# Kernel tuning notes

Hardware: AMD Instinct MI355X
Metric: run time of the kernel (lower is better)

The kernel has to match this reference:

```python
import jax, jax.numpy as jnp
import numpy as np

XLIM = 10.0
N_BINS = 200
LATTICE = 12.42
N_O, N_H = 64, 128
T, R = 1000, 8


def setup_inputs() -> dict:
    key = jax.random.key(0)
    k1, k2 = jax.random.split(key)
    n = N_O + N_H
    stacked_radii = jax.random.uniform(k1, (T, R, n, 3), dtype=jnp.float32) * LATTICE
    lattices = jnp.full((3,), LATTICE, dtype=jnp.float32)
    gt_rdf = jax.random.uniform(k2, (3, N_BINS), dtype=jnp.float32)
    idx_O = jnp.arange(N_O, dtype=jnp.int32)
    idx_H = jnp.arange(N_H, dtype=jnp.int32) + N_O
    return {"stacked_radii": stacked_radii, "lattices": lattices,
            "gt_rdf": gt_rdf, "idx_O": idx_O, "idx_H": idx_H}


def reference(stacked_radii, lattices, gt_rdf, idx_O, idx_H):
    bins = jnp.linspace(1e-6, XLIM, N_BINS + 1, dtype=jnp.float32)
    # np.histogram normalization: rho * (4/3)pi (r_hi^3 - r_lo^3)
    shell = (4.0 / 3.0) * np.pi * (bins[1:] ** 3 - bins[:-1] ** 3)
    vol = jnp.prod(lattices)
    # wrap positions into the box (data_seq / L % 1 * L)
    x = stacked_radii / lattices % 1.0 * lattices
    x = jnp.transpose(x, (1, 0, 2, 3))  # [R, T, N, 3]

    def pair_rdf(x_rep, i0, i1):
        x0 = x_rep[:, i0]  # [T, n0, 3]
        x1 = x_rep[:, i1]  # [T, n1, 3]
        # all-pairs minimum-image distance under PBC
        delta = jnp.abs(x0[:, :, None, :] - x1[:, None, :, :])  # [T, n0, n1, 3]
        delta = jnp.where(delta > 0.5 * lattices, delta - lattices, delta)
        d = jnp.sqrt(jnp.sum(delta ** 2, axis=-1)).ravel()
        n_pairs = d.shape[0]  # includes zeros, matches original rho
        mask = (d != 0.0) & (d >= bins[0]) & (d <= bins[-1])
        bidx = jnp.clip(jnp.searchsorted(bins, d, side='right') - 1, 0, N_BINS - 1)
        hist = jax.ops.segment_sum(mask.astype(jnp.float32), bidx, num_segments=N_BINS)
        rho = n_pairs / vol
        return hist / (rho * shell)  # [N_BINS]

    pairs = [(idx_O, idx_O), (idx_H, idx_H), (idx_H, idx_O)]  # OO, HH, HO
    # sequential over replicas (like the original python loop) to bound memory
    rdfs = [jax.lax.map(lambda xr, i0=i0, i1=i1: pair_rdf(xr, i0, i1), x)
            for (i0, i1) in pairs]  # each [R, N_BINS]
    maes = jnp.stack([XLIM * jnp.mean(jnp.abs(r - g), axis=-1)
                      for r, g in zip(rdfs, gt_rdf)], axis=0)  # [3, R]
    max_maes = jnp.max(maes, axis=0)  # [R]
    rdf_stack = jnp.concatenate(rdfs, axis=-1)  # [R, 3*N_BINS]
    return rdf_stack, max_maes
```

## Files before the change

kernel.cpp:

```cpp
#include <hip/hip_runtime.h>
#include <math.h>

#define NUM_T   1000
#define NUM_R   8
#define NBINS   200
#define FPB     2
#define TTSZ    224
#define TYSTR   218
#define NCOL    8
#define HWORDS  2616

__device__ __forceinline__ float approx_sqrt(float x) {
    float r; asm("v_sqrt_f32 %0, %1" : "=v"(r) : "v"(x)); return r;
}
__device__ __forceinline__ float fract_(float x) {
#if __has_builtin(__builtin_amdgcn_fractf)
    return __builtin_amdgcn_fractf(x);
#else
    return x - floorf(x);
#endif
}

__global__ __launch_bounds__(256) void rdf_hist_kernel(
    const float* __restrict__ radii,
    const float* __restrict__ lat,
    unsigned int* __restrict__ gh)
{
    #pragma clang fp contract(off)
    __shared__ float4 posOx[96], posH0[96], posH1[96];
    __shared__ float TT[TTSZ];
    __shared__ unsigned int hist[HWORDS];

    const int tid = threadIdx.x;

    if (tid < TTSZ) {
        float v;
        if (tid <= 200) {
            float b;
            if (tid < NBINS) {
                const double step = (10.0 - 1e-6) / 200.0;
                b = (float)(1e-6 + (double)tid * step);
            } else {
                b = __uint_as_float(__float_as_uint(10.0f) + 1u);
            }
            unsigned lo = 0u, hi = 0x7F800000u;
            while (lo < hi) {
                unsigned mid = (lo + hi) >> 1;
                if (sqrtf(__uint_as_float(mid)) >= b) hi = mid; else lo = mid + 1;
            }
            v = __uint_as_float(lo);
        } else {
            v = __uint_as_float(0x7F800000u);
        }
        TT[tid] = v;
    }
    for (int i = tid; i < HWORDS; i += 256) hist[i] = 0u;

    const float Lx = lat[0], Ly = lat[1], Lz = lat[2];
    __syncthreads();

    const int col = tid & (NCOL - 1);

#define PAIR(PI, PJ, TBASE, W)                                               \
    {                                                                        \
        float tx = (PI).x - (PJ).x;                                          \
        float ty = (PI).y - (PJ).y;                                          \
        float tz = (PI).z - (PJ).z;                                          \
        float ax = fminf(fabsf(tx), Lx - fabsf(tx));                         \
        float ay = fminf(fabsf(ty), Ly - fabsf(ty));                         \
        float az = fminf(fabsf(tz), Lz - fabsf(tz));                         \
        float s  = (ax*ax + ay*ay) + az*az;                                  \
        float z  = approx_sqrt(s * 400.0f);                                  \
        int   k  = (int)z;                                                   \
        float m  = fract_(z);                                                \
        bool amb = fabsf(m - 0.5f) > 0.49980f;                               \
        if (__builtin_expect(__any(amb), 0)) {                               \
            float tlo = TT[k], thi = TT[k + 1];                              \
            k += ((s >= thi) ? 1 : 0) - ((s < tlo) ? 1 : 0);                 \
            if (k < 0) k = 216;                                              \
        }                                                                    \
        int w = (TBASE) + ((k >> 1) << 3);                                   \
        unsigned val = (unsigned)(W) << ((k & 1) << 4);                      \
        atomicAdd(&hist[w], val);                                            \
    }

    const int rep   = blockIdx.x & (NUM_R - 1);
    const int chunk = blockIdx.x / NUM_R;
    const int l     = tid & 63;
    const int q     = tid >> 6;
    const int tbOO  = col;
    const int tbHH  = col + 109 * NCOL;
    const int tbHO  = col + 218 * NCOL;

    float rvx = 0.f, rvy = 0.f, rvz = 0.f;
    {
        const float* s0 = radii + ((size_t)(chunk * FPB) * NUM_R + rep) * (192 * 3);
        if (tid < 192) { rvx = s0[tid*3+0]; rvy = s0[tid*3+1]; rvz = s0[tid*3+2]; }
    }

    #pragma unroll 1
    for (int f = 0; f < FPB; ++f) {
        __syncthreads();
        if (tid < 192) {
            float ux = rvx / Lx; ux -= floorf(ux);
            float uy = rvy / Ly; uy -= floorf(uy);
            float uz = rvz / Lz; uz -= floorf(uz);
            float4 p = make_float4(ux*Lx, uy*Ly, uz*Lz, 0.0f);
            if (tid < 64)       { posOx[tid] = p;  if (tid < 32) posOx[tid+64] = p; }
            else if (tid < 128) { int h = tid-64;  posH0[h] = p; if (h < 32) posH0[h+64] = p; }
            else                { int h = tid-128; posH1[h] = p; if (h < 32) posH1[h+64] = p; }
        }
        __syncthreads();

        if (f + 1 < FPB && tid < 192) {
            const float* s1 = radii + ((size_t)(chunk * FPB + f + 1) * NUM_R + rep) * (192 * 3);
            rvx = s1[tid*3+0]; rvy = s1[tid*3+1]; rvz = s1[tid*3+2];
        }

        const float4 piO = posOx[l];
        const float4 pi0 = posH0[l];
        const float4 pi1 = posH1[l];
        const int jb = l + q + 1;

        #pragma unroll
        for (int it = 0; it < 7; ++it) { float4 pj = posOx[jb + 4*it]; PAIR(piO, pj, tbOO, 2u); }
        if (q < 3 || l < 32)           { float4 pj = posOx[jb + 28];   PAIR(piO, pj, tbOO, 2u); }

        #pragma unroll
        for (int it = 0; it < 7; ++it) { float4 pj = posH0[jb + 4*it]; PAIR(pi0, pj, tbHH, 2u); }
        if (q < 3 || l < 32)           { float4 pj = posH0[jb + 28];   PAIR(pi0, pj, tbHH, 2u); }

        #pragma unroll
        for (int it = 0; it < 7; ++it) { float4 pj = posH1[jb + 4*it]; PAIR(pi1, pj, tbHH, 2u); }
        if (q < 3 || l < 32)           { float4 pj = posH1[jb + 28];   PAIR(pi1, pj, tbHH, 2u); }

        #pragma unroll 4
        for (int jj = 0; jj < 16; ++jj) {
            float4 pj = posH1[q * 16 + jj];
            PAIR(pi0, pj, tbHH, 2u);
        }
        #pragma unroll 4
        for (int jj = 0; jj < 16; ++jj) {
            float4 pj = posOx[q * 16 + jj];
            PAIR(pi0, pj, tbHO, 1u);
            PAIR(pi1, pj, tbHO, 1u);
        }
    }
#undef PAIR

    __syncthreads();
    for (int idx = tid; idx < 3 * NBINS; idx += 256) {
        const int p    = idx / 200;
        const int b    = idx - p * 200;
        const int pr   = p * TYSTR + b;
        const int base = (pr >> 1) << 3;
        const int sh   = (b & 1) << 4;
        const int c0   = idx & (NCOL - 1);
        unsigned sum = 0;
        #pragma unroll
        for (int c = 0; c < NCOL; ++c) {
            unsigned wrd = hist[base + ((c0 + c) & (NCOL - 1))];
            sum += (wrd >> sh) & 0xFFFFu;
        }
        if (sum) atomicAdd(&gh[rep * 3 * NBINS + idx], sum);
    }
}

__global__ __launch_bounds__(256) void rdf_final_kernel(
    const unsigned int* __restrict__ gh,
    const float* __restrict__ gt,
    const float* __restrict__ lat,
    float* __restrict__ out)
{
    #pragma clang fp contract(off)
    const int rep = blockIdx.x;
    const int tid = threadIdx.x;
    __shared__ float bins[NBINS + 1];
    __shared__ float red[256];

    for (int i = tid; i <= NBINS; i += 256) {
        const double step = (10.0 - 1e-6) / 200.0;
        bins[i] = (i == NBINS) ? 10.0f : (float)(1e-6 + (double)i * step);
    }
    __syncthreads();

    const float vol = (lat[0] * lat[1]) * lat[2];
    const float C   = 4.18879020478639053f;
    const int npairs[3] = { NUM_T*64*64, NUM_T*128*128, NUM_T*128*64 };

    float maxmae = -3.0e38f;
    for (int p = 0; p < 3; ++p) {
        float diff = 0.0f;
        if (tid < NBINS) {
            float b0 = bins[tid], b1 = bins[tid + 1];
            float shell = C * (b1*b1*b1 - b0*b0*b0);
            float rho = (float)npairs[p] / vol;
            float g = (float)gh[(rep*3 + p)*NBINS + tid] / (rho * shell);
            out[rep*3*NBINS + p*NBINS + tid] = g;
            diff = fabsf(g - gt[p*NBINS + tid]);
        }
        red[tid] = diff;
        __syncthreads();
        for (int s = 128; s > 0; s >>= 1) {
            if (tid < s) red[tid] += red[tid + s];
            __syncthreads();
        }
        if (tid == 0) {
            float mae = 10.0f * (red[0] / 200.0f);
            if (mae > maxmae) maxmae = mae;
        }
        __syncthreads();
    }
    if (tid == 0) out[NUM_R*3*NBINS + rep] = maxmae;
}

extern "C" void kernel_launch(void* const* d_in, const int* in_sizes, int n_in,
                              void* d_out, int out_size, void* d_ws, size_t ws_size,
                              hipStream_t stream) {
    const float* radii = (const float*)d_in[0];
    const float* lat   = (const float*)d_in[1];
    const float* gt    = (const float*)d_in[2];
    unsigned int* gh   = (unsigned int*)d_ws;

    hipMemsetAsync(gh, 0, NUM_R * 3 * NBINS * sizeof(unsigned int), stream);

    dim3 grid(NUM_R * (NUM_T / FPB));
    hipLaunchKernelGGL(rdf_hist_kernel, grid, dim3(256), 0, stream,
                       radii, lat, gh);
    hipLaunchKernelGGL(rdf_final_kernel, dim3(NUM_R), dim3(256), 0, stream,
                       gh, gt, lat, (float*)d_out);
}
```

Before: 101.0 us.

## Use 32-bit histogram words with fewer copies and readlane broadcast for cross pairs

Replaces the packed 16-bit-per-bin, 8-copy shared histogram with full 32-bit counters, one per bin, replicated in 4 column copies. This removes the shift/mask packing and lets the final reduction read one uint4 per bin. The cross-pair loops (H0-H1 and H-O) now take the j-particle coordinates from registers with readlane broadcasts instead of LDS loads, using a wave-uniform q. Fewer histogram copies may raise LDS atomic contention, in exchange for simpler address arithmetic and less LDS traffic.

```diff
diff --git a/kernel.cpp b/kernel.cpp
--- a/kernel.cpp
+++ b/kernel.cpp
@@ -6,9 +6,9 @@
 #define NBINS   200
 #define FPB     2
 #define TTSZ    224
-#define TYSTR   218
-#define NCOL    8
-#define HWORDS  2616
+#define TYSTR   217
+#define NCOL    4
+#define HWORDS  (3*TYSTR*NCOL)
 
 __device__ __forceinline__ float approx_sqrt(float x) {
     float r; asm("v_sqrt_f32 %0, %1" : "=v"(r) : "v"(x)); return r;
@@ -19,6 +19,9 @@
 #else
     return x - floorf(x);
 #endif
+}
+__device__ __forceinline__ float rlanef(float v, int sidx) {
+    return __uint_as_float(__builtin_amdgcn_readlane(__float_as_uint(v), sidx));
 }
 
 __global__ __launch_bounds__(256) void rdf_hist_kernel(
@@ -29,7 +32,7 @@
     #pragma clang fp contract(off)
     __shared__ float4 posOx[96], posH0[96], posH1[96];
     __shared__ float TT[TTSZ];
-    __shared__ unsigned int hist[HWORDS];
+    __shared__ __align__(16) unsigned int hist[HWORDS];
 
     const int tid = threadIdx.x;
 
@@ -61,11 +64,8 @@
 
     const int col = tid & (NCOL - 1);
 
-#define PAIR(PI, PJ, TBASE, W)                                               \
+#define PTAIL(TB, W)                                                         \
     {                                                                        \
-        float tx = (PI).x - (PJ).x;                                          \
-        float ty = (PI).y - (PJ).y;                                          \
-        float tz = (PI).z - (PJ).z;                                          \
         float ax = fminf(fabsf(tx), Lx - fabsf(tx));                         \
         float ay = fminf(fabsf(ty), Ly - fabsf(ty));                         \
         float az = fminf(fabsf(tz), Lz - fabsf(tz));                         \
@@ -79,18 +79,32 @@
             k += ((s >= thi) ? 1 : 0) - ((s < tlo) ? 1 : 0);                 \
             if (k < 0) k = 216;                                              \
         }                                                                    \
-        int w = (TBASE) + ((k >> 1) << 3);                                   \
-        unsigned val = (unsigned)(W) << ((k & 1) << 4);                      \
-        atomicAdd(&hist[w], val);                                            \
+        atomicAdd(&hist[(TB) + (k << 2)], (W));                              \
+    }
+
+#define PAIRV(PI, PJ, TB, W)                                                 \
+    {                                                                        \
+        float tx = (PI).x - (PJ).x;                                          \
+        float ty = (PI).y - (PJ).y;                                          \
+        float tz = (PI).z - (PJ).z;                                          \
+        PTAIL(TB, W)                                                         \
+    }
+#define PAIRS(PI, SX, SY, SZ, TB, W)                                         \
+    {                                                                        \
+        float tx = (PI).x - (SX);                                            \
+        float ty = (PI).y - (SY);                                            \
+        float tz = (PI).z - (SZ);                                            \
+        PTAIL(TB, W)                                                         \
     }
 
     const int rep   = blockIdx.x & (NUM_R - 1);
     const int chunk = blockIdx.x / NUM_R;
     const int l     = tid & 63;
     const int q     = tid >> 6;
+    const int qu    = __builtin_amdgcn_readfirstlane(q);
     const int tbOO  = col;
-    const int tbHH  = col + 109 * NCOL;
-    const int tbHO  = col + 218 * NCOL;
+    const int tbHH  = col + (TYSTR << 2);
+    const int tbHO  = col + (2 * TYSTR << 2);
 
     float rvx = 0.f, rvy = 0.f, rvz = 0.f;
     {
@@ -123,45 +137,41 @@
         const int jb = l + q + 1;
 
         #pragma unroll
-        for (int it = 0; it < 7; ++it) { float4 pj = posOx[jb + 4*it]; PAIR(piO, pj, tbOO, 2u); }
-        if (q < 3 || l < 32)           { float4 pj = posOx[jb + 28];   PAIR(piO, pj, tbOO, 2u); }
+        for (int it = 0; it < 7; ++it) { float4 pj = posOx[jb + 4*it]; PAIRV(piO, pj, tbOO, 2u); }
+        if (q < 3 || l < 32)           { float4 pj = posOx[jb + 28];   PAIRV(piO, pj, tbOO, 2u); }
 
         #pragma unroll
-        for (int it = 0; it < 7; ++it) { float4 pj = posH0[jb + 4*it]; PAIR(pi0, pj, tbHH, 2u); }
-        if (q < 3 || l < 32)           { float4 pj = posH0[jb + 28];   PAIR(pi0, pj, tbHH, 2u); }
+        for (int it = 0; it < 7; ++it) { float4 pj = posH0[jb + 4*it]; PAIRV(pi0, pj, tbHH, 2u); }
+        if (q < 3 || l < 32)           { float4 pj = posH0[jb + 28];   PAIRV(pi0, pj, tbHH, 2u); }
 
         #pragma unroll
-        for (int it = 0; it < 7; ++it) { float4 pj = posH1[jb + 4*it]; PAIR(pi1, pj, tbHH, 2u); }
-        if (q < 3 || l < 32)           { float4 pj = posH1[jb + 28];   PAIR(pi1, pj, tbHH, 2u); }
+        for (int it = 0; it < 7; ++it) { float4 pj = posH1[jb + 4*it]; PAIRV(pi1, pj, tbHH, 2u); }
+        if (q < 3 || l < 32)           { float4 pj = posH1[jb + 28];   PAIRV(pi1, pj, tbHH, 2u); }
 
         #pragma unroll 4
         for (int jj = 0; jj < 16; ++jj) {
-            float4 pj = posH1[q * 16 + jj];
-            PAIR(pi0, pj, tbHH, 2u);
+            const int idx = qu * 16 + jj;
+            float sx = rlanef(pi1.x, idx), sy = rlanef(pi1.y, idx), sz = rlanef(pi1.z, idx);
+            PAIRS(pi0, sx, sy, sz, tbHH, 2u);
         }
         #pragma unroll 4
         for (int jj = 0; jj < 16; ++jj) {
-            float4 pj = posOx[q * 16 + jj];
-            PAIR(pi0, pj, tbHO, 1u);
-            PAIR(pi1, pj, tbHO, 1u);
-        }
-    }
-#undef PAIR
+            const int idx = qu * 16 + jj;
+            float sx = rlanef(piO.x, idx), sy = rlanef(piO.y, idx), sz = rlanef(piO.z, idx);
+            PAIRS(pi0, sx, sy, sz, tbHO, 1u);
+            PAIRS(pi1, sx, sy, sz, tbHO, 1u);
+        }
+    }
+#undef PAIRV
+#undef PAIRS
+#undef PTAIL
 
     __syncthreads();
     for (int idx = tid; idx < 3 * NBINS; idx += 256) {
-        const int p    = idx / 200;
-        const int b    = idx - p * 200;
-        const int pr   = p * TYSTR + b;
-        const int base = (pr >> 1) << 3;
-        const int sh   = (b & 1) << 4;
-        const int c0   = idx & (NCOL - 1);
-        unsigned sum = 0;
-        #pragma unroll
-        for (int c = 0; c < NCOL; ++c) {
-            unsigned wrd = hist[base + ((c0 + c) & (NCOL - 1))];
-            sum += (wrd >> sh) & 0xFFFFu;
-        }
+        const int p = idx / 200;
+        const int b = idx - p * 200;
+        const uint4 v = *reinterpret_cast<const uint4*>(&hist[(p * TYSTR + b) << 2]);
+        unsigned sum = (v.x + v.y) + (v.z + v.w);
         if (sum) atomicAdd(&gh[rep * 3 * NBINS + idx], sum);
     }
 }
```

Measured after the change: 104.8 us. +3.7%, slower.
